# Kernel tuning notes

Hardware: AMD Instinct MI355X
Metric: run time of the kernel (lower is better)

Reference implementation:

```python
import jax, jax.numpy as jnp
import numpy as np

N, E = 50000, 800000          # nodes, edges (avg degree 16)
D_IN, D_H = 128, 128          # input_size, hidden_size


def setup_inputs() -> dict:
    key = jax.random.key(0)
    ks = jax.random.split(key, 10)
    s = 0.05  # param init scale
    return {
        "x": jax.random.normal(ks[0], (N, D_IN), jnp.float32),
        "edge_index": jax.random.randint(ks[1], (2, E), 0, N, jnp.int32),
        "h_prev": jax.random.normal(ks[2], (N, D_H), jnp.float32),
        # reset gate params: xr (Linear with bias), hr (no bias)
        "W_xr": jax.random.normal(ks[3], (D_IN, D_H), jnp.float32) * s,
        "b_xr": jnp.zeros((D_H,), jnp.float32),
        "W_hr": jax.random.normal(ks[4], (D_H, D_H), jnp.float32) * s,
        # update gate params
        "W_xz": jax.random.normal(ks[5], (D_IN, D_H), jnp.float32) * s,
        "b_xz": jnp.zeros((D_H,), jnp.float32),
        "W_hz": jax.random.normal(ks[6], (D_H, D_H), jnp.float32) * s,
        # SAGEConv params: lin_l on mean-aggregated neighbors (bias), lin_r on root (no bias)
        "W_l": jax.random.normal(ks[7], (D_IN + D_H, D_H), jnp.float32) * s,
        "b_l": jnp.zeros((D_H,), jnp.float32),
        "W_r": jax.random.normal(ks[8], (D_IN + D_H, D_H), jnp.float32) * s,
    }


def reference(x, edge_index, h_prev, W_xr, b_xr, W_hr, W_xz, b_xz, W_hz, W_l, b_l, W_r):
    # GRU-style gates
    r = jax.nn.sigmoid(x @ W_xr + b_xr + h_prev @ W_hr)   # [N, D_H]
    z = jax.nn.sigmoid(x @ W_xz + b_xz + h_prev @ W_hz)   # [N, D_H]

    # candidate via single-layer GraphSAGE (SAGEConv, mean aggregation)
    xc = jnp.concatenate([x, r * h_prev], axis=-1)        # [N, D_IN+D_H]
    src, dst = edge_index[0], edge_index[1]
    agg = jax.ops.segment_sum(xc[src], dst, num_segments=N)              # [N, D_IN+D_H]
    cnt = jax.ops.segment_sum(jnp.ones((E,), xc.dtype), dst, num_segments=N)
    mean_nbr = agg / jnp.maximum(cnt, 1.0)[:, None]
    # PyG BasicGNN applies no activation after the last (only) layer, so no tanh here.
    n = mean_nbr @ W_l + b_l + xc @ W_r                   # [N, D_H]

    return (1.0 - z) * n + z * h_prev
```

## Files before the change

### kernel.cpp

```cpp
#include <hip/hip_runtime.h>
#include <hip/hip_bf16.h>

typedef __attribute__((ext_vector_type(8))) short bf16x8;
typedef __attribute__((ext_vector_type(4))) short s16x4;
typedef __attribute__((ext_vector_type(4))) float f32x4;
typedef __attribute__((ext_vector_type(4))) int i32x4;
typedef unsigned short u16;
typedef unsigned int u32;

#define D 128
#define DC 256
#define TILES 8
#define NPART 8
#define SWZ(row, dim) (((row) << 7) + ((dim) ^ (((row) & 15) << 3)))

__device__ __forceinline__ float bf2f(u16 b) {
    u32 u = ((u32)b) << 16;
    return __uint_as_float(u);
}
__device__ __forceinline__ u16 f2bf(float f) {
    u32 u = __float_as_uint(f);
    u32 r = (u + 0x7fffu + ((u >> 16) & 1u)) >> 16;
    return (u16)r;
}
__device__ __forceinline__ float sigmoidf_(float x) {
    float e = __builtin_amdgcn_exp2f(-1.4426950408889634f * x);
    return __builtin_amdgcn_rcpf(1.0f + e);
}
__device__ __forceinline__ bf16x8 cvt8(const float* __restrict__ p) {
    f32x4 lo = *(const f32x4*)p;
    f32x4 hi = *(const f32x4*)(p + 4);
    union { bf16x8 v; u16 s[8]; } u;
#pragma unroll
    for (int i = 0; i < 4; i++) {
        u.s[i]     = f2bf(lo[i]);
        u.s[i + 4] = f2bf(hi[i]);
    }
    return u.v;
}

__global__ __launch_bounds__(256) void prep_kernel(
    const float* __restrict__ Wxr, const float* __restrict__ Whr,
    const float* __restrict__ Wxz, const float* __restrict__ Whz,
    const float* __restrict__ Wl,  const float* __restrict__ Wr,
    u16* __restrict__ WxrT, u16* __restrict__ WhrT,
    u16* __restrict__ WxzT, u16* __restrict__ WhzT,
    u16* __restrict__ WlT,  u16* __restrict__ WrT,
    const int* __restrict__ ei, int* __restrict__ deg,
    int E)
{
    int bid = blockIdx.x;
    int tid = threadIdx.x;
    if (bid < 64) {
        int m = bid >> 4;
        int idx = (bid & 15) * 1024 + tid * 4;
        const float* W = (m == 0) ? Wxr : (m == 1) ? Whr : (m == 2) ? Wxz : Whz;
        u16* Wt        = (m == 0) ? WxrT : (m == 1) ? WhrT : (m == 2) ? WxzT : WhzT;
        f32x4 v = *(const f32x4*)(W + idx);
        int k = idx >> 7, n = idx & 127;
#pragma unroll
        for (int j = 0; j < 4; j++) Wt[(n + j) * D + k] = f2bf(v[j]);
    } else if (bid < 128) {
        int m = (bid - 64) >> 5;
        int idx = ((bid - 64) & 31) * 1024 + tid * 4;
        const float* W = (m == 0) ? Wl : Wr;
        u16* Wt        = (m == 0) ? WlT : WrT;
        f32x4 v = *(const f32x4*)(W + idx);
        int k = idx >> 7, n = idx & 127;
#pragma unroll
        for (int j = 0; j < 4; j++) Wt[(n + j) * DC + k] = f2bf(v[j]);
    } else {
        long long e = ((long long)(bid - 128) * 256 + tid) * 4;
        if (e + 3 < E) {
            i32x4 d4 = *(const i32x4*)(ei + (size_t)E + e);
#pragma unroll
            for (int j = 0; j < 4; j++) atomicAdd(&deg[d4[j]], 1);
        } else {
            for (int j = 0; j < 4 && e + j < E; j++)
                atomicAdd(&deg[ei[(size_t)E + e + j]], 1);
        }
    }
}

__global__ __launch_bounds__(256) void scan1_kernel(
    const int* __restrict__ deg, int* __restrict__ rstart,
    int* __restrict__ bsum, int N)
{
    __shared__ int tmp[256];
    int t = threadIdx.x;
    int g = blockIdx.x * 256 + t;
    int v = (g < N) ? deg[g] : 0;
    tmp[t] = v;
    __syncthreads();
#pragma unroll
    for (int s = 1; s < 256; s <<= 1) {
        int add = (t >= s) ? tmp[t - s] : 0;
        __syncthreads();
        tmp[t] += add;
        __syncthreads();
    }
    if (g < N) rstart[g] = tmp[t] - v;
    if (t == 255) bsum[blockIdx.x] = tmp[255];
}

__global__ __launch_bounds__(256) void scan23_kernel(
    int* __restrict__ rstart, const int* __restrict__ bsum, int N, int nbn)
{
    __shared__ int tmp[256];
    int t = threadIdx.x;
    int v = (t < nbn) ? bsum[t] : 0;
    tmp[t] = v;
    __syncthreads();
#pragma unroll
    for (int s = 1; s < 256; s <<= 1) {
        int add = (t >= s) ? tmp[t - s] : 0;
        __syncthreads();
        tmp[t] += add;
        __syncthreads();
    }
    int b = blockIdx.x;
    int excl = tmp[b] - ((b < nbn) ? bsum[b] : 0);
    int g = b * 256 + t;
    if (g < N) rstart[g] += excl;
}

__global__ __launch_bounds__(256) void fill_kernel(
    const int* __restrict__ ei, int* __restrict__ rstart,
    int* __restrict__ col, int E, int SL, int PSTEP)
{
    const int part = blockIdx.x & (NPART - 1);
    const int sidx = blockIdx.x >> 3;
    const int lo = part * PSTEP, hi = lo + PSTEP;
    long long base = (long long)sidx * SL;
    long long end  = base + SL; if (end > E) end = E;
    for (long long e = base + threadIdx.x * 4; e < end; e += 1024) {
        if (e + 4 <= end) {
            i32x4 s4 = *(const i32x4*)(ei + e);
            i32x4 d4 = *(const i32x4*)(ei + (size_t)E + e);
#pragma unroll
            for (int j = 0; j < 4; j++) {
                int dd = d4[j];
                if (dd >= lo && dd < hi) {
                    int pos = atomicAdd(&rstart[dd], 1);
                    col[pos] = s4[j];
                }
            }
        } else {
            for (long long q = e; q < end; q++) {
                int dd = ei[(size_t)E + q];
                if (dd >= lo && dd < hi) {
                    int pos = atomicAdd(&rstart[dd], 1);
                    col[pos] = ei[q];
                }
            }
        }
    }
}

__global__ __launch_bounds__(512, 4) void fused_kernel(
    const float* __restrict__ x, const float* __restrict__ h,
    const u16* __restrict__ WxrT, const u16* __restrict__ WhrT,
    const u16* __restrict__ WxzT, const u16* __restrict__ WhzT,
    const u16* __restrict__ WlT,  const u16* __restrict__ WrT,
    const float* __restrict__ bxr, const float* __restrict__ bxz,
    u16* __restrict__ zo, u16* __restrict__ yo, u16* __restrict__ wo, int N)
{
    __shared__ u16 xT[TILES][16 * 128];
    __shared__ u16 hT[TILES][16 * 128];
    const int wave = threadIdx.x >> 6;
    const int lane = threadIdx.x & 63;
    const int quad = lane >> 4;
    const int l15  = lane & 15;
    const int node0 = blockIdx.x * (TILES * 16);
    if (node0 >= N) return;

    {
        int tb = node0 + wave * 16;
        u16* Lx = xT[wave];
        u16* Lh = hT[wave];
#pragma unroll
        for (int it = 0; it < 4; it++) {
            int idx = it * 64 + lane;
            int row = idx >> 4, seg = idx & 15;
            int node = tb + row; if (node >= N) node = N - 1;
            *(bf16x8*)&Lx[SWZ(row, seg * 8)] = cvt8(x + (size_t)node * D + seg * 8);
            *(bf16x8*)&Lh[SWZ(row, seg * 8)] = cvt8(h + (size_t)node * D + seg * 8);
        }
    }
    __syncthreads();

    const int dim = wave * 16 + l15;
    u32 rhp0[TILES], rhp1[TILES];

    {
        const u16* wrx = WxrT + (size_t)dim * D + quad * 8;
        const u16* wrh = WhrT + (size_t)dim * D + quad * 8;
        const u16* wzx = WxzT + (size_t)dim * D + quad * 8;
        const u16* wzh = WhzT + (size_t)dim * D + quad * 8;
        bf16x8 b0[4], b1[4], b2[4], b3[4];
#pragma unroll
        for (int c = 0; c < 4; c++) {
            b0[c] = *(const bf16x8*)(wrx + c * 32);
            b1[c] = *(const bf16x8*)(wrh + c * 32);
            b2[c] = *(const bf16x8*)(wzx + c * 32);
            b3[c] = *(const bf16x8*)(wzh + c * 32);
        }
        float br = bxr[dim];
        float bz = bxz[dim];
#pragma unroll
        for (int t = 0; t < TILES; t++) {
            const u16* Lx = xT[t];
            const u16* Lh = hT[t];
            int tb = node0 + t * 16;
            bf16x8 ax[4], ah[4];
#pragma unroll
            for (int c = 0; c < 4; c++) {
                ax[c] = *(const bf16x8*)&Lx[SWZ(l15, c * 32 + quad * 8)];
                ah[c] = *(const bf16x8*)&Lh[SWZ(l15, c * 32 + quad * 8)];
            }
            f32x4 ar = {0.f,0.f,0.f,0.f};
            f32x4 az = {0.f,0.f,0.f,0.f};
#pragma unroll
            for (int c = 0; c < 4; c++) {
                ar = __builtin_amdgcn_mfma_f32_16x16x32_bf16(ax[c], b0[c], ar, 0, 0, 0);
                ar = __builtin_amdgcn_mfma_f32_16x16x32_bf16(ah[c], b1[c], ar, 0, 0, 0);
                az = __builtin_amdgcn_mfma_f32_16x16x32_bf16(ax[c], b2[c], az, 0, 0, 0);
                az = __builtin_amdgcn_mfma_f32_16x16x32_bf16(ah[c], b3[c], az, 0, 0, 0);
            }
            u32 p0 = 0, p1 = 0;
#pragma unroll
            for (int reg = 0; reg < 4; reg++) {
                int row = quad * 4 + reg;
                int node = tb + row;
                float hv = bf2f(Lh[SWZ(row, dim)]);
                float r  = sigmoidf_(ar[reg] + br);
                float zz = sigmoidf_(az[reg] + bz);
                u32 rh = f2bf(r * hv);
                if (reg == 0) p0 = rh;
                else if (reg == 1) p0 |= rh << 16;
                else if (reg == 2) p1 = rh;
                else p1 |= rh << 16;
                if (node < N) zo[(size_t)node * D + dim] = f2bf(zz);
            }
            rhp0[t] = p0;
            rhp1[t] = p1;
        }
    }
    __syncthreads();

#pragma unroll
    for (int t = 0; t < TILES; t++) {
        u16* Lh = hT[t];
        Lh[SWZ(quad * 4 + 0, dim)] = (u16)(rhp0[t]);
        Lh[SWZ(quad * 4 + 1, dim)] = (u16)(rhp0[t] >> 16);
        Lh[SWZ(quad * 4 + 2, dim)] = (u16)(rhp1[t]);
        Lh[SWZ(quad * 4 + 3, dim)] = (u16)(rhp1[t] >> 16);
    }
    __syncthreads();

    {
        const u16* pl = WlT + (size_t)dim * DC + quad * 8;
        const u16* pr = WrT + (size_t)dim * DC + quad * 8;
        bf16x8 l0[4], l1[4], r0[4], r1[4];
#pragma unroll
        for (int c = 0; c < 4; c++) {
            l0[c] = *(const bf16x8*)(pl + c * 32);
            l1[c] = *(const bf16x8*)(pl + 128 + c * 32);
            r0[c] = *(const bf16x8*)(pr + c * 32);
            r1[c] = *(const bf16x8*)(pr + 128 + c * 32);
        }
#pragma unroll
        for (int t = 0; t < TILES; t++) {
            const u16* Lx  = xT[t];
            const u16* Lrh = hT[t];
            int tb = node0 + t * 16;
            bf16x8 ax[4], arh[4];
#pragma unroll
            for (int c = 0; c < 4; c++) {
                ax[c]  = *(const bf16x8*)&Lx[SWZ(l15, c * 32 + quad * 8)];
                arh[c] = *(const bf16x8*)&Lrh[SWZ(l15, c * 32 + quad * 8)];
            }
            f32x4 ay = {0.f,0.f,0.f,0.f};
            f32x4 aw = {0.f,0.f,0.f,0.f};
#pragma unroll
            for (int c = 0; c < 4; c++) {
                ay = __builtin_amdgcn_mfma_f32_16x16x32_bf16(ax[c],  l0[c], ay, 0, 0, 0);
                ay = __builtin_amdgcn_mfma_f32_16x16x32_bf16(arh[c], l1[c], ay, 0, 0, 0);
                aw = __builtin_amdgcn_mfma_f32_16x16x32_bf16(ax[c],  r0[c], aw, 0, 0, 0);
                aw = __builtin_amdgcn_mfma_f32_16x16x32_bf16(arh[c], r1[c], aw, 0, 0, 0);
            }
#pragma unroll
            for (int reg = 0; reg < 4; reg++) {
                int row = quad * 4 + reg;
                int node = tb + row;
                if (node < N) {
                    yo[(size_t)node * D + dim] = f2bf(ay[reg]);
                    wo[(size_t)node * D + dim] = f2bf(aw[reg]);
                }
            }
        }
    }
}

__global__ __launch_bounds__(256) void pull_kernel(
    const int* __restrict__ rend, const int* __restrict__ deg,
    const int* __restrict__ col, const u16* __restrict__ y,
    const u16* __restrict__ z, const u16* __restrict__ w,
    const float* __restrict__ h, const float* __restrict__ bl,
    float* __restrict__ out, int N)
{
    const int wave = threadIdx.x >> 6;
    const int lane = threadIdx.x & 63;
    const int node = blockIdx.x * 4 + wave;
    if (node >= N) return;

    const int d    = deg[node];
    const int base = rend[node] - d;
    const int g    = lane >> 4;
    const int l15  = lane & 15;

    const int dcap = (d < 64) ? d : 64;
    int cols = 0;
    if (lane < dcap) cols = col[base + lane];

    float a[8] = {0.f,0.f,0.f,0.f,0.f,0.f,0.f,0.f};
    for (int i = 0; i < dcap; i += 8) {
        int e0 = i + g, e1 = i + 4 + g;
        int s0 = __shfl(cols, e0 & 63, 64);
        int s1 = __shfl(cols, e1 & 63, 64);
        bool v0 = e0 < dcap, v1 = e1 < dcap;
        bf16x8 A = {}, B = {};
        if (v0) A = *(const bf16x8*)(y + (size_t)s0 * D + l15 * 8);
        if (v1) B = *(const bf16x8*)(y + (size_t)s1 * D + l15 * 8);
        if (v0) {
#pragma unroll
            for (int j = 0; j < 8; j++) a[j] += bf2f((u16)A[j]);
        }
        if (v1) {
#pragma unroll
            for (int j = 0; j < 8; j++) a[j] += bf2f((u16)B[j]);
        }
    }
    for (int i = 64; i < d; i += 4) {
        int e = i + g;
        if (e < d) {
            int s = col[base + e];
            bf16x8 v = *(const bf16x8*)(y + (size_t)s * D + l15 * 8);
#pragma unroll
            for (int j = 0; j < 8; j++) a[j] += bf2f((u16)v[j]);
        }
    }
#pragma unroll
    for (int j = 0; j < 8; j++) {
        a[j] += __shfl_xor(a[j], 16, 64);
        a[j] += __shfl_xor(a[j], 32, 64);
    }
    if (lane < 16) {
        float inv = 1.0f / (float)(d > 0 ? d : 1);
        size_t o16 = (size_t)node * D + l15 * 8;
        bf16x8 zv = *(const bf16x8*)(z + o16);
        bf16x8 wv = *(const bf16x8*)(w + o16);
        f32x4 h0 = *(const f32x4*)(h + o16);
        f32x4 h1 = *(const f32x4*)(h + o16 + 4);
        f32x4 b0 = *(const f32x4*)(bl + l15 * 8);
        f32x4 b1 = *(const f32x4*)(bl + l15 * 8 + 4);
        f32x4 o0, o1;
#pragma unroll
        for (int j = 0; j < 4; j++) {
            float zz = bf2f((u16)zv[j]);
            float nv = a[j] * inv + b0[j] + bf2f((u16)wv[j]);
            o0[j] = (1.0f - zz) * nv + zz * h0[j];
        }
#pragma unroll
        for (int j = 0; j < 4; j++) {
            float zz = bf2f((u16)zv[j + 4]);
            float nv = a[j + 4] * inv + b1[j] + bf2f((u16)wv[j + 4]);
            o1[j] = (1.0f - zz) * nv + zz * h1[j];
        }
        *(f32x4*)(out + o16)     = o0;
        *(f32x4*)(out + o16 + 4) = o1;
    }
}

extern "C" void kernel_launch(void* const* d_in, const int* in_sizes, int n_in,
                              void* d_out, int out_size, void* d_ws, size_t ws_size,
                              hipStream_t stream)
{
    const float* x   = (const float*)d_in[0];
    const int*   ei  = (const int*)d_in[1];
    const float* h   = (const float*)d_in[2];
    const float* Wxr = (const float*)d_in[3];
    const float* bxr = (const float*)d_in[4];
    const float* Whr = (const float*)d_in[5];
    const float* Wxz = (const float*)d_in[6];
    const float* bxz = (const float*)d_in[7];
    const float* Whz = (const float*)d_in[8];
    const float* Wl  = (const float*)d_in[9];
    const float* bl  = (const float*)d_in[10];
    const float* Wr  = (const float*)d_in[11];
    float* out = (float*)d_out;

    const int N = in_sizes[0] / D;
    const int E = in_sizes[1] / 2;
    if (N <= 0 || E <= 0) return;

    const int nbn = (N + 255) / 256;
    if (nbn > 256) return;

    char* ws = (char*)d_ws;
    size_t off = 0;
    auto alloc = [&](size_t bytes) -> void* {
        void* p = ws + off;
        off += (bytes + 255) & ~(size_t)255;
        return p;
    };
    u16*   z     = (u16*)  alloc((size_t)N * D * 2);
    u16*   y     = (u16*)  alloc((size_t)N * D * 2);
    u16*   w     = (u16*)  alloc((size_t)N * D * 2);
    int*   deg   = (int*)  alloc((size_t)N * 4);
    int*   rstart= (int*)  alloc((size_t)N * 4);
    int*   bsum  = (int*)  alloc((size_t)256 * 4);
    int*   col   = (int*)  alloc((size_t)E * 4);
    u16*   WxrT  = (u16*)  alloc((size_t)D * D * 2);
    u16*   WhrT  = (u16*)  alloc((size_t)D * D * 2);
    u16*   WxzT  = (u16*)  alloc((size_t)D * D * 2);
    u16*   WhzT  = (u16*)  alloc((size_t)D * D * 2);
    u16*   WlT   = (u16*)  alloc((size_t)DC * D * 2);
    u16*   WrT   = (u16*)  alloc((size_t)DC * D * 2);
    (void)n_in; (void)out_size;
    if (off > ws_size) return;

    hipMemsetAsync(deg, 0, (size_t)N * 4, stream);

    const int nbh4 = (E + 1023) / 1024;
    prep_kernel<<<128 + nbh4, 256, 0, stream>>>(
        Wxr, Whr, Wxz, Whz, Wl, Wr,
        WxrT, WhrT, WxzT, WhzT, WlT, WrT,
        ei, deg, E);

    scan1_kernel<<<nbn, 256, 0, stream>>>(deg, rstart, bsum, N);
    scan23_kernel<<<nbn, 256, 0, stream>>>(rstart, bsum, N, nbn);

    const int nsl   = 98;
    const int SL    = (((E + nsl - 1) / nsl) + 3) & ~3;
    const int PSTEP = (N + NPART - 1) / NPART;
    fill_kernel<<<NPART * nsl, 256, 0, stream>>>(ei, rstart, col, E, SL, PSTEP);

    fused_kernel<<<(N + TILES * 16 - 1) / (TILES * 16), 512, 0, stream>>>(
        x, h, WxrT, WhrT, WxzT, WhzT, WlT, WrT, bxr, bxz, z, y, w, N);

    pull_kernel<<<(N + 3) / 4, 256, 0, stream>>>(
        rstart, deg, col, y, z, w, h, bl, out, N);
}
```

Before: 274.0 us.

## Merge two-pass degree scan into single-pass decoupled-lookback scan; shrink fused tile count

Replaces the two scan kernels with one kernel that passes block prefix sums through a tagged state array (decoupled lookback), removing one launch and one pass over rstart. The memset now also zeroes the state array. Separately, TILES drops from 8 to 6, so each fused block handles fewer nodes and uses less shared memory, which gives more blocks. The launch still uses 512 threads, so two waves per block are guarded off the load, leaving possible idle waves. The lookback spin relies on predecessor blocks being scheduled, which holds for about 196 blocks.

```diff
diff --git a/kernel.cpp b/kernel.cpp
--- a/kernel.cpp
+++ b/kernel.cpp
@@ -7,10 +7,11 @@
 typedef __attribute__((ext_vector_type(4))) int i32x4;
 typedef unsigned short u16;
 typedef unsigned int u32;
+typedef unsigned long long u64;
 
 #define D 128
 #define DC 256
-#define TILES 8
+#define TILES 6
 #define NPART 8
 #define SWZ(row, dim) (((row) << 7) + ((dim) ^ (((row) & 15) << 3)))
 
@@ -82,13 +83,15 @@
     }
 }
 
-__global__ __launch_bounds__(256) void scan1_kernel(
+__global__ __launch_bounds__(256) void scan_kernel(
     const int* __restrict__ deg, int* __restrict__ rstart,
-    int* __restrict__ bsum, int N)
+    u64* __restrict__ state, int N)
 {
     __shared__ int tmp[256];
-    int t = threadIdx.x;
-    int g = blockIdx.x * 256 + t;
+    __shared__ int s_excl;
+    const int c = blockIdx.x;
+    const int t = threadIdx.x;
+    int g = c * 256 + t;
     int v = (g < N) ? deg[g] : 0;
     tmp[t] = v;
     __syncthreads();
@@ -99,29 +102,33 @@
         tmp[t] += add;
         __syncthreads();
     }
-    if (g < N) rstart[g] = tmp[t] - v;
-    if (t == 255) bsum[blockIdx.x] = tmp[255];
-}
-
-__global__ __launch_bounds__(256) void scan23_kernel(
-    int* __restrict__ rstart, const int* __restrict__ bsum, int N, int nbn)
-{
-    __shared__ int tmp[256];
-    int t = threadIdx.x;
-    int v = (t < nbn) ? bsum[t] : 0;
-    tmp[t] = v;
+    int total = tmp[255];
+    if (t == 0) {
+        if (c == 0) {
+            __hip_atomic_store(&state[0], (2ull << 32) | (u32)total,
+                               __ATOMIC_RELEASE, __HIP_MEMORY_SCOPE_AGENT);
+            s_excl = 0;
+        } else {
+            __hip_atomic_store(&state[c], (1ull << 32) | (u32)total,
+                               __ATOMIC_RELEASE, __HIP_MEMORY_SCOPE_AGENT);
+            long long sum = 0;
+            int j = c - 1;
+            while (j >= 0) {
+                u64 s = __hip_atomic_load(&state[j],
+                        __ATOMIC_ACQUIRE, __HIP_MEMORY_SCOPE_AGENT);
+                u32 tag = (u32)(s >> 32);
+                if (tag == 0) continue;
+                sum += (u32)s;
+                if (tag == 2) break;
+                j--;
+            }
+            s_excl = (int)sum;
+            __hip_atomic_store(&state[c], (2ull << 32) | (u32)(sum + total),
+                               __ATOMIC_RELEASE, __HIP_MEMORY_SCOPE_AGENT);
+        }
+    }
     __syncthreads();
-#pragma unroll
-    for (int s = 1; s < 256; s <<= 1) {
-        int add = (t >= s) ? tmp[t - s] : 0;
-        __syncthreads();
-        tmp[t] += add;
-        __syncthreads();
-    }
-    int b = blockIdx.x;
-    int excl = tmp[b] - ((b < nbn) ? bsum[b] : 0);
-    int g = b * 256 + t;
-    if (g < N) rstart[g] += excl;
+    if (g < N) rstart[g] = s_excl + tmp[t] - v;
 }
 
 __global__ __launch_bounds__(256) void fill_kernel(
@@ -174,7 +181,7 @@
     const int node0 = blockIdx.x * (TILES * 16);
     if (node0 >= N) return;
 
-    {
+    if (wave < TILES) {
         int tb = node0 + wave * 16;
         u16* Lx = xT[wave];
         u16* Lh = hT[wave];
@@ -418,8 +425,8 @@
     u16*   y     = (u16*)  alloc((size_t)N * D * 2);
     u16*   w     = (u16*)  alloc((size_t)N * D * 2);
     int*   deg   = (int*)  alloc((size_t)N * 4);
+    u64*   state = (u64*)  alloc((size_t)256 * 8);
     int*   rstart= (int*)  alloc((size_t)N * 4);
-    int*   bsum  = (int*)  alloc((size_t)256 * 4);
     int*   col   = (int*)  alloc((size_t)E * 4);
     u16*   WxrT  = (u16*)  alloc((size_t)D * D * 2);
     u16*   WhrT  = (u16*)  alloc((size_t)D * D * 2);
@@ -430,7 +437,7 @@
     (void)n_in; (void)out_size;
     if (off > ws_size) return;
 
-    hipMemsetAsync(deg, 0, (size_t)N * 4, stream);
+    hipMemsetAsync(deg, 0, (size_t)((char*)rstart - (char*)deg), stream);
 
     const int nbh4 = (E + 1023) / 1024;
     prep_kernel<<<128 + nbh4, 256, 0, stream>>>(
@@ -438,8 +445,7 @@
         WxrT, WhrT, WxzT, WhzT, WlT, WrT,
         ei, deg, E);
 
-    scan1_kernel<<<nbn, 256, 0, stream>>>(deg, rstart, bsum, N);
-    scan23_kernel<<<nbn, 256, 0, stream>>>(rstart, bsum, N, nbn);
+    scan_kernel<<<nbn, 256, 0, stream>>>(deg, rstart, state, N);
 
     const int nsl   = 98;
     const int SL    = (((E + nsl - 1) / nsl) + 3) & ~3;
```

Result: slower. 315.7 us (+15.2%).
